# Kernel optimization log

Measured on AMD Instinct MI355X. Metric: run time of the kernel, lower is better.

The kernel has to match this reference:

```python
import jax, jax.numpy as jnp
import numpy as np

B, S, D, H = 2, 2048, 1024, 16
DEPTH = D // H
NEG = -1.0e9


def setup_inputs() -> dict:
    key = jax.random.key(0)
    ks = jax.random.split(key, 12)
    scale = 1.0 / np.sqrt(D)
    inp = {
        "k": jax.random.normal(ks[0], (B, S, D), jnp.float32),
        "v": jax.random.normal(ks[1], (B, S, D), jnp.float32),
        "q": jax.random.normal(ks[2], (B, S, D), jnp.float32),
        # causal mask: 1 where attention is disallowed (j > i)
        "mask": jnp.triu(jnp.ones((S, S), jnp.float32), k=1),
        "wq_w": jax.random.normal(ks[3], (D, D), jnp.float32) * scale,
        "wq_b": jnp.zeros((D,), jnp.float32),
        "wk_w": jax.random.normal(ks[4], (D, D), jnp.float32) * scale,
        "wk_b": jnp.zeros((D,), jnp.float32),
        "wv_w": jax.random.normal(ks[5], (D, D), jnp.float32) * scale,
        "wv_b": jnp.zeros((D,), jnp.float32),
        "wo_w": jax.random.normal(ks[6], (D, D), jnp.float32) * scale,
        "wo_b": jnp.zeros((D,), jnp.float32),
    }
    return inp


def _split_heads(x):
    # [B, S, D] -> [B, H, S, depth]
    return x.reshape(B, S, H, DEPTH).transpose(0, 2, 1, 3)


def reference(k, v, q, mask, wq_w, wq_b, wk_w, wk_b, wv_w, wv_b, wo_w, wo_b):
    qh = _split_heads(q @ wq_w + wq_b)
    kh = _split_heads(k @ wk_w + wk_b)
    vh = _split_heads(v @ wv_w + wv_b)
    # scaled dot-product attention with additive mask
    logits = jnp.einsum("bhsd,bhtd->bhst", qh, kh) / jnp.sqrt(
        jnp.asarray(DEPTH, jnp.float32)
    )
    logits = logits + mask * NEG  # mask broadcasts over [B, H]
    attn = jax.nn.softmax(logits, axis=-1)
    ctx = jnp.einsum("bhst,bhtd->bhsd", attn, vh)
    concat = ctx.transpose(0, 2, 1, 3).reshape(B, S, D)
    out = concat @ wo_w + wo_b
    return out, attn
```

## Files before the change

kernel.cpp:

```cpp
#include <hip/hip_runtime.h>
#include <hip/hip_bf16.h>
#include <stdint.h>

typedef __attribute__((ext_vector_type(8))) short bf16x8;
typedef __attribute__((ext_vector_type(4))) float f32x4;
typedef __attribute__((ext_vector_type(4))) unsigned short u16x4;
typedef unsigned short u16;

#define GLD16(g, l) __builtin_amdgcn_global_load_lds( \
    (const __attribute__((address_space(1))) unsigned int*)(g), \
    (__attribute__((address_space(3))) unsigned int*)(l), 16, 0, 0)

__device__ __forceinline__ u16 f2bf(float f) {
  union { __hip_bfloat16 h; u16 u; } cv;
  cv.h = __float2bfloat16(f);
  return cv.u;
}

__global__ __launch_bounds__(256) void convert_kernel(
    const float* __restrict__ s0, const float* __restrict__ s1,
    const float* __restrict__ s2,
    u16* __restrict__ d0, u16* __restrict__ d1, u16* __restrict__ d2) {
  const int z = blockIdx.y;
  const float* s = (z == 0) ? s0 : (z == 1) ? s1 : s2;
  u16* d = (z == 0) ? d0 : (z == 1) ? d1 : d2;
  const int n4 = (2 * 2048 * 1024) / 4;
  for (int i = blockIdx.x * 256 + threadIdx.x; i < n4; i += gridDim.x * 256) {
    float4 v = ((const float4*)s)[i];
    u16x4 o = {f2bf(v.x), f2bf(v.y), f2bf(v.z), f2bf(v.w)};
    ((u16x4*)d)[i] = o;
  }
}

__global__ __launch_bounds__(256) void transw_kernel(
    const float* __restrict__ w0, const float* __restrict__ w1,
    const float* __restrict__ w2, const float* __restrict__ w3,
    u16* __restrict__ o0, u16* __restrict__ o1,
    u16* __restrict__ o2, u16* __restrict__ o3) {
  __shared__ float t[64][65];
  const int z = blockIdx.z;
  const float* w = (z == 0) ? w0 : (z == 1) ? w1 : (z == 2) ? w2 : w3;
  u16* o = (z == 0) ? o0 : (z == 1) ? o1 : (z == 2) ? o2 : o3;
  const int bi = blockIdx.x * 64, bj = blockIdx.y * 64;
  const int c = threadIdx.x & 63, r0 = threadIdx.x >> 6;
#pragma unroll
  for (int i = 0; i < 16; i++) {
    int r = r0 + i * 4;
    t[r][c] = w[(size_t)(bi + r) * 1024 + bj + c];
  }
  __syncthreads();
#pragma unroll
  for (int i = 0; i < 16; i++) {
    int r = r0 + i * 4;
    o[(size_t)(bj + r) * 1024 + bi + c] = f2bf(t[c][r]);
  }
}

static __device__ __forceinline__ void gemm_mainloop(
    const u16* __restrict__ A, const u16* __restrict__ Bt, int bm, int bn,
    u16* Ash, u16* Bsh, f32x4 (&acc)[4][4]) {
  const int tid = threadIdx.x;
  const int wave = tid >> 6, lane = tid & 63;
  const int wm = (wave >> 1) * 64, wn = (wave & 1) * 64;
  const f32x4 vzero = {0.f, 0.f, 0.f, 0.f};
#pragma unroll
  for (int mi = 0; mi < 4; mi++)
#pragma unroll
    for (int ni = 0; ni < 4; ni++) acc[mi][ni] = vzero;

  for (int k0 = 0; k0 < 1024; k0 += 64) {
    __syncthreads();
#pragma unroll
    for (int i = 0; i < 4; i++) {
      int t = i * 256 + tid;
      int row = t >> 3;
      int colb = ((t & 7) * 16) ^ ((row & 7) << 4);
      GLD16((const char*)A + ((size_t)(bm + row) * 1024 + k0) * 2 + colb,
            (char*)Ash + (i * 256 + wave * 64) * 16);
    }
#pragma unroll
    for (int i = 0; i < 4; i++) {
      int t = i * 256 + tid;
      int row = t >> 3;
      int colb = ((t & 7) * 16) ^ ((row & 7) << 4);
      GLD16((const char*)Bt + ((size_t)(bn + row) * 1024 + k0) * 2 + colb,
            (char*)Bsh + (i * 256 + wave * 64) * 16);
    }
    __syncthreads();
#pragma unroll
    for (int kk = 0; kk < 2; kk++) {
      const int d0 = kk * 32 + (lane >> 4) * 8;
      bf16x8 af[4], bv[4];
#pragma unroll
      for (int mi = 0; mi < 4; mi++) {
        int r = wm + mi * 16 + (lane & 15);
        af[mi] = *(const bf16x8*)((const char*)Ash + r * 128 +
                                  ((d0 * 2) ^ ((r & 7) << 4)));
      }
#pragma unroll
      for (int ni = 0; ni < 4; ni++) {
        int r = wn + ni * 16 + (lane & 15);
        bv[ni] = *(const bf16x8*)((const char*)Bsh + r * 128 +
                                  ((d0 * 2) ^ ((r & 7) << 4)));
      }
#pragma unroll
      for (int mi = 0; mi < 4; mi++)
#pragma unroll
        for (int ni = 0; ni < 4; ni++)
          acc[mi][ni] = __builtin_amdgcn_mfma_f32_16x16x32_bf16(
              af[mi], bv[ni], acc[mi][ni], 0, 0, 0);
    }
  }
}

__global__ __launch_bounds__(256) void proj3_kernel(
    const u16* __restrict__ xq, const u16* __restrict__ xk,
    const u16* __restrict__ xv, const u16* __restrict__ wqT,
    const u16* __restrict__ wkT, const u16* __restrict__ wvT,
    const float* __restrict__ bq, const float* __restrict__ bk,
    const float* __restrict__ bv, u16* __restrict__ Qh, u16* __restrict__ Kh,
    u16* __restrict__ Vt) {
  __shared__ u16 Ash[128 * 64], Bsh[128 * 64];
  const int z = blockIdx.z;
  const u16* A = (z == 0) ? xq : (z == 1) ? xk : xv;
  const u16* Bt = (z == 0) ? wqT : (z == 1) ? wkT : wvT;
  const float* bias = (z == 0) ? bq : (z == 1) ? bk : bv;
  const int bm = blockIdx.x * 128, bn = blockIdx.y * 128;
  f32x4 acc[4][4];
  gemm_mainloop(A, Bt, bm, bn, Ash, Bsh, acc);
  const int lane = threadIdx.x & 63, wave = threadIdx.x >> 6;
  const int wm = (wave >> 1) * 64, wn = (wave & 1) * 64;
#pragma unroll
  for (int ni = 0; ni < 4; ni++) {
    int gn = bn + wn + ni * 16 + (lane & 15);
    float bb = bias[gn];
#pragma unroll
    for (int mi = 0; mi < 4; mi++) {
#pragma unroll
      for (int j = 0; j < 4; j++) {
        int gm = bm + wm + mi * 16 + (lane >> 4) * 4 + j;
        float c = acc[mi][ni][j] + bb;
        if (z < 2) {
          u16* o = (z == 0) ? Qh : Kh;
          o[(size_t)gm * 1024 + gn] = f2bf(c);
        } else {
          int b = gm >> 11, s = gm & 2047, hh = gn >> 6, d = gn & 63;
          Vt[(((size_t)b * 16 + hh) * 64 + d) * 2048 + s] = f2bf(c);
        }
      }
    }
  }
}

__global__ __launch_bounds__(256) void gemm_out_kernel(
    const u16* __restrict__ A, const u16* __restrict__ Bt,
    const float* __restrict__ bias, float* __restrict__ out) {
  __shared__ u16 Ash[128 * 64], Bsh[128 * 64];
  const int bm = blockIdx.x * 128, bn = blockIdx.y * 128;
  f32x4 acc[4][4];
  gemm_mainloop(A, Bt, bm, bn, Ash, Bsh, acc);
  const int lane = threadIdx.x & 63, wave = threadIdx.x >> 6;
  const int wm = (wave >> 1) * 64, wn = (wave & 1) * 64;
#pragma unroll
  for (int ni = 0; ni < 4; ni++) {
    int gn = bn + wn + ni * 16 + (lane & 15);
    float bb = bias[gn];
#pragma unroll
    for (int mi = 0; mi < 4; mi++) {
#pragma unroll
      for (int j = 0; j < 4; j++) {
        int gm = bm + wm + mi * 16 + (lane >> 4) * 4 + j;
        out[(size_t)gm * 1024 + gn] = acc[mi][ni][j] + bb;
      }
    }
  }
}

__global__ __launch_bounds__(256) void attn_kernel(
    const u16* __restrict__ Qh, const u16* __restrict__ Kh,
    const u16* __restrict__ Vt, float* __restrict__ attn,
    u16* __restrict__ concat) {
  const int bid = blockIdx.x;
  const int xcd = bid & 7;
  const int r = bid >> 3;
  const int qt = 31 - (r & 31);
  const int hb = xcd * 4 + (r >> 5);
  const int h = hb & 15, b = hb >> 4;
  const int tid = threadIdx.x, wave = tid >> 6, lane = tid & 63;
  const int l15 = lane & 15, lhi = lane >> 4;
  const f32x4 vzero = {0.f, 0.f, 0.f, 0.f};

  __shared__ u16 Ksh[2][64 * 64], Vsh[2][64 * 64];
  __shared__ float Psf[4][1024];
  char* Pwc = (char*)Psf[wave];

  const u16* Kbase = Kh + (size_t)(b * 2048) * 1024 + h * 64;
  const u16* Vbase = Vt + (size_t)(b * 16 + h) * 64 * 2048;
  float* attn_bh = attn + (size_t)(b * 16 + h) * 2048 * 2048;

  auto stageK = [&](u16* dst, int kt) {
#pragma unroll
    for (int i = 0; i < 2; i++) {
      int t = i * 256 + tid;
      int row = t >> 3;
      int colb = ((t & 7) * 16) ^ ((row & 7) << 4);
      GLD16((const char*)(Kbase + (size_t)(kt * 64 + row) * 1024) + colb,
            (char*)dst + (i * 256 + wave * 64) * 16);
    }
  };
  auto stageV = [&](u16* dst, int kt) {
#pragma unroll
    for (int i = 0; i < 2; i++) {
      int t = i * 256 + tid;
      int row = t >> 3;
      int colb = ((t & 7) * 16) ^ ((row & 7) << 4);
      GLD16((const char*)(Vbase + (size_t)row * 2048 + kt * 64) + colb,
            (char*)dst + (i * 256 + wave * 64) * 16);
    }
  };
  auto qkt = [&](const u16* Kbuf, const bf16x8* qf, f32x4* sacc) {
#pragma unroll
    for (int ni = 0; ni < 4; ni++) sacc[ni] = vzero;
    __builtin_amdgcn_s_setprio(1);
#pragma unroll
    for (int kk = 0; kk < 2; kk++) {
      const int d0 = kk * 32 + lhi * 8;
#pragma unroll
      for (int ni = 0; ni < 4; ni++) {
        int r2 = ni * 16 + l15;
        bf16x8 kf = *(const bf16x8*)((const char*)Kbuf + r2 * 128 +
                                     ((d0 * 2) ^ ((r2 & 7) << 4)));
        sacc[ni] = __builtin_amdgcn_mfma_f32_16x16x32_bf16(qf[kk], kf,
                                                           sacc[ni], 0, 0, 0);
      }
    }
    __builtin_amdgcn_s_setprio(0);
  };

  const u16* Qrow =
      Qh + (size_t)(b * 2048 + qt * 64 + wave * 16 + l15) * 1024 + h * 64;
  bf16x8 qf[2];
  qf[0] = *(const bf16x8*)(Qrow + lhi * 8);
  qf[1] = *(const bf16x8*)(Qrow + 32 + lhi * 8);

  float srow[4] = {0.f, 0.f, 0.f, 0.f};
  stageK(Ksh[0], 0);
  __syncthreads();
  int cur = 0;
  for (int kt = 0; kt <= qt; kt++) {
    if (kt < qt) stageK(Ksh[cur ^ 1], kt + 1);
    f32x4 sacc[4];
    qkt(Ksh[cur], qf, sacc);
#pragma unroll
    for (int j = 0; j < 4; j++) {
      const int gi = qt * 64 + wave * 16 + lhi * 4 + j;
      float ps = 0.f;
#pragma unroll
      for (int ni = 0; ni < 4; ni++) {
        int gj = kt * 64 + ni * 16 + l15;
        float l = fminf(sacc[ni][j] * 0.125f, 60.f);
        ps += (gj > gi) ? 0.f : __expf(l);
      }
#pragma unroll
      for (int dd = 1; dd < 16; dd <<= 1) ps += __shfl_xor(ps, dd, 16);
      srow[j] += ps;
    }
    __syncthreads();
    cur ^= 1;
  }
  float rs[4];
#pragma unroll
  for (int j = 0; j < 4; j++) rs[j] = 1.0f / srow[j];

  f32x4 ctx[4];
#pragma unroll
  for (int ni = 0; ni < 4; ni++) ctx[ni] = vzero;
  stageK(Ksh[0], 0);
  stageV(Vsh[0], 0);
  __syncthreads();
  cur = 0;
  for (int kt = 0; kt <= qt; kt++) {
    if (kt < qt) {
      stageK(Ksh[cur ^ 1], kt + 1);
      stageV(Vsh[cur ^ 1], kt + 1);
    }
    f32x4 sacc[4];
    qkt(Ksh[cur], qf, sacc);
#pragma unroll
    for (int j = 0; j < 4; j++) {
      const int riw = lhi * 4 + j;
      const int gi = qt * 64 + wave * 16 + riw;
#pragma unroll
      for (int ni = 0; ni < 4; ni++) {
        const int cj = ni * 16 + l15;
        const int gj = kt * 64 + cj;
        float l = fminf(sacc[ni][j] * 0.125f, 60.f);
        float p = (gj > gi) ? 0.f : __expf(l) * rs[j];
        *(float*)(Pwc + ((riw * 256 + cj * 4) ^ ((riw & 7) << 4))) = p;
      }
    }
    asm volatile("s_waitcnt lgkmcnt(0)" ::: "memory");
    __builtin_amdgcn_sched_barrier(0);
#pragma unroll
    for (int s = 0; s < 4; s++) {
      const int row = s * 4 + lhi;
      const int gi = qt * 64 + wave * 16 + row;
      f32x4 pv4 =
          *(const f32x4*)(Pwc + ((row * 256 + l15 * 16) ^ ((row & 7) << 4)));
      __builtin_nontemporal_store(
          pv4, (f32x4*)(attn_bh + (size_t)gi * 2048 + kt * 64 + l15 * 4));
    }
    __builtin_amdgcn_s_setprio(1);
#pragma unroll
    for (int kk = 0; kk < 2; kk++) {
      const int s0 = kk * 32 + lhi * 8;
      f32x4 pa = *(const f32x4*)(Pwc +
                                 ((l15 * 256 + s0 * 4) ^ ((l15 & 7) << 4)));
      f32x4 pb = *(const f32x4*)(
          Pwc + ((l15 * 256 + s0 * 4 + 16) ^ ((l15 & 7) << 4)));
      bf16x8 pf;
      pf[0] = (short)f2bf(pa.x); pf[1] = (short)f2bf(pa.y);
      pf[2] = (short)f2bf(pa.z); pf[3] = (short)f2bf(pa.w);
      pf[4] = (short)f2bf(pb.x); pf[5] = (short)f2bf(pb.y);
      pf[6] = (short)f2bf(pb.z); pf[7] = (short)f2bf(pb.w);
#pragma unroll
      for (int ni = 0; ni < 4; ni++) {
        int vr = ni * 16 + l15;
        bf16x8 vf = *(const bf16x8*)((const char*)Vsh[cur] + vr * 128 +
                                     ((s0 * 2) ^ ((vr & 7) << 4)));
        ctx[ni] = __builtin_amdgcn_mfma_f32_16x16x32_bf16(pf, vf, ctx[ni],
                                                          0, 0, 0);
      }
    }
    __builtin_amdgcn_s_setprio(0);
    asm volatile("s_waitcnt vmcnt(4) lgkmcnt(0)" ::: "memory");
    __builtin_amdgcn_sched_barrier(0);
    __builtin_amdgcn_s_barrier();
    cur ^= 1;
  }

#pragma unroll
  for (int ni = 0; ni < 4; ni++) {
#pragma unroll
    for (int j = 0; j < 4; j++) {
      int gm = b * 2048 + qt * 64 + wave * 16 + lhi * 4 + j;
      int gn = h * 64 + ni * 16 + l15;
      concat[(size_t)gm * 1024 + gn] = f2bf(ctx[ni][j]);
    }
  }

  const int zc0 = (qt + 1) * 64;
  if (zc0 < 2048) {
    const f32x4 z4 = {0.f, 0.f, 0.f, 0.f};
    const int W4 = (2048 - zc0) >> 2;
    f32x4* rowbase = (f32x4*)(attn_bh + (size_t)(qt * 64) * 2048 + zc0);
    for (int rr = 0; rr < 64; rr++) {
      f32x4* rp = rowbase + (size_t)rr * 512;
      for (int cc = tid; cc < W4; cc += 256)
        __builtin_nontemporal_store(z4, &rp[cc]);
    }
  }
}

extern "C" void kernel_launch(void* const* d_in, const int* in_sizes, int n_in,
                              void* d_out, int out_size, void* d_ws,
                              size_t ws_size, hipStream_t stream) {
  const float* k_in = (const float*)d_in[0];
  const float* v_in = (const float*)d_in[1];
  const float* q_in = (const float*)d_in[2];
  const float* wq_w = (const float*)d_in[4];
  const float* wq_b = (const float*)d_in[5];
  const float* wk_w = (const float*)d_in[6];
  const float* wk_b = (const float*)d_in[7];
  const float* wv_w = (const float*)d_in[8];
  const float* wv_b = (const float*)d_in[9];
  const float* wo_w = (const float*)d_in[10];
  const float* wo_b = (const float*)d_in[11];

  char* ws = (char*)d_ws;
  u16* xq = (u16*)(ws + ((size_t)0 << 20));
  u16* xk = (u16*)(ws + ((size_t)8 << 20));
  u16* xv = (u16*)(ws + ((size_t)16 << 20));
  u16* wqT = (u16*)(ws + ((size_t)24 << 20));
  u16* wkT = (u16*)(ws + ((size_t)26 << 20));
  u16* wvT = (u16*)(ws + ((size_t)28 << 20));
  u16* woT = (u16*)(ws + ((size_t)30 << 20));
  u16* Qh = (u16*)(ws + ((size_t)32 << 20));
  u16* Kh = (u16*)(ws + ((size_t)40 << 20));
  u16* Vt = (u16*)(ws + ((size_t)48 << 20));
  u16* concat = (u16*)(ws + ((size_t)56 << 20));

  float* outp = (float*)d_out;
  float* attnp = outp + (size_t)2 * 2048 * 1024;

  convert_kernel<<<dim3(512, 3), dim3(256), 0, stream>>>(q_in, k_in, v_in, xq,
                                                         xk, xv);
  transw_kernel<<<dim3(16, 16, 4), dim3(256), 0, stream>>>(
      wq_w, wk_w, wv_w, wo_w, wqT, wkT, wvT, woT);
  proj3_kernel<<<dim3(32, 8, 3), dim3(256), 0, stream>>>(
      xq, xk, xv, wqT, wkT, wvT, wq_b, wk_b, wv_b, Qh, Kh, Vt);
  attn_kernel<<<dim3(1024), dim3(256), 0, stream>>>(Qh, Kh, Vt, attnp, concat);
  gemm_out_kernel<<<dim3(32, 8), dim3(256), 0, stream>>>(concat, woT, wo_b,
                                                         outp);
}
```

Before: 231.3 us.

## Move causal-mask zero-fill of attention output into projection and output GEMMs

```diff
diff --git a/kernel.cpp b/kernel.cpp
--- a/kernel.cpp
+++ b/kernel.cpp
@@ -15,6 +15,28 @@
   union { __hip_bfloat16 h; u16 u; } cv;
   cv.h = __float2bfloat16(f);
   return cv.u;
+}
+
+__device__ __forceinline__ void zerofill_units(float* __restrict__ attn_all,
+                                               int u0, int u1, int stride,
+                                               int tid) {
+  const f32x4 z4 = {0.f, 0.f, 0.f, 0.f};
+  for (int u = u0; u < u1; u += stride) {
+    int bh = u / 496;
+    int rem = u - bh * 496;
+    int i = 0;
+    while (rem >= 31 - i) { rem -= 31 - i; i++; }
+    int j = i + 1 + rem;
+    float* base = attn_all + (size_t)bh * 2048 * 2048 +
+                  (size_t)(i * 64) * 2048 + j * 64;
+#pragma unroll
+    for (int t = 0; t < 4; t++) {
+      int idx = t * 256 + tid;
+      int row = idx >> 4, c4 = idx & 15;
+      __builtin_nontemporal_store(z4,
+                                  (f32x4*)(base + (size_t)row * 2048 + c4 * 4));
+    }
+  }
 }
 
 __global__ __launch_bounds__(256) void convert_kernel(
@@ -119,7 +141,7 @@
     const u16* __restrict__ wkT, const u16* __restrict__ wvT,
     const float* __restrict__ bq, const float* __restrict__ bk,
     const float* __restrict__ bv, u16* __restrict__ Qh, u16* __restrict__ Kh,
-    u16* __restrict__ Vt) {
+    u16* __restrict__ Vt, float* __restrict__ attn_all) {
   __shared__ u16 Ash[128 * 64], Bsh[128 * 64];
   const int z = blockIdx.z;
   const u16* A = (z == 0) ? xq : (z == 1) ? xk : xv;
@@ -150,11 +172,14 @@
       }
     }
   }
+  const int bid = blockIdx.x + blockIdx.y * 32 + z * 256;
+  zerofill_units(attn_all, bid, 10752, 768, threadIdx.x);
 }
 
 __global__ __launch_bounds__(256) void gemm_out_kernel(
     const u16* __restrict__ A, const u16* __restrict__ Bt,
-    const float* __restrict__ bias, float* __restrict__ out) {
+    const float* __restrict__ bias, float* __restrict__ out,
+    float* __restrict__ attn_all) {
   __shared__ u16 Ash[128 * 64], Bsh[128 * 64];
   const int bm = blockIdx.x * 128, bn = blockIdx.y * 128;
   f32x4 acc[4][4];
@@ -174,6 +199,8 @@
       }
     }
   }
+  const int bid = blockIdx.x + blockIdx.y * 32;
+  zerofill_units(attn_all, 10752 + bid, 15872, 256, threadIdx.x);
 }
 
 __global__ __launch_bounds__(256) void attn_kernel(
@@ -346,18 +373,6 @@
       int gm = b * 2048 + qt * 64 + wave * 16 + lhi * 4 + j;
       int gn = h * 64 + ni * 16 + l15;
       concat[(size_t)gm * 1024 + gn] = f2bf(ctx[ni][j]);
-    }
-  }
-
-  const int zc0 = (qt + 1) * 64;
-  if (zc0 < 2048) {
-    const f32x4 z4 = {0.f, 0.f, 0.f, 0.f};
-    const int W4 = (2048 - zc0) >> 2;
-    f32x4* rowbase = (f32x4*)(attn_bh + (size_t)(qt * 64) * 2048 + zc0);
-    for (int rr = 0; rr < 64; rr++) {
-      f32x4* rp = rowbase + (size_t)rr * 512;
-      for (int cc = tid; cc < W4; cc += 256)
-        __builtin_nontemporal_store(z4, &rp[cc]);
     }
   }
 }
@@ -398,8 +413,8 @@
   transw_kernel<<<dim3(16, 16, 4), dim3(256), 0, stream>>>(
       wq_w, wk_w, wv_w, wo_w, wqT, wkT, wvT, woT);
   proj3_kernel<<<dim3(32, 8, 3), dim3(256), 0, stream>>>(
-      xq, xk, xv, wqT, wkT, wvT, wq_b, wk_b, wv_b, Qh, Kh, Vt);
+      xq, xk, xv, wqT, wkT, wvT, wq_b, wk_b, wv_b, Qh, Kh, Vt, attnp);
   attn_kernel<<<dim3(1024), dim3(256), 0, stream>>>(Qh, Kh, Vt, attnp, concat);
   gemm_out_kernel<<<dim3(32, 8), dim3(256), 0, stream>>>(concat, woT, wo_b,
-                                                         outp);
-}
+                                                         outp, attnp);
+}
```

Result: slower. 240.4 us (+3.9%).
